# Kernel tuning notes

Hardware: AMD Instinct MI355X
Metric: run time of the kernel (lower is better)

Reference implementation:

```python
import jax, jax.numpy as jnp
import numpy as np

B, S, H = 128, 4096, 128

def setup_inputs() -> dict:
    key = jax.random.key(0)
    k1, k2, k3, k4 = jax.random.split(key, 4)
    x = jax.random.normal(k1, (B, S, H), dtype=jnp.float32)
    # nn.Linear default init ~ U(-1/sqrt(H), 1/sqrt(H)); values don't affect correctness checks
    lim = 1.0 / np.sqrt(H)
    W = jax.random.uniform(k2, (H, H), dtype=jnp.float32, minval=-lim, maxval=lim)
    b = jax.random.uniform(k3, (H,), dtype=jnp.float32, minval=-lim, maxval=lim)
    v = jax.random.uniform(k4, (H,), dtype=jnp.float32, minval=-0.1, maxval=0.1)
    return {"x": x, "W": W, "b": b, "v": v}

def reference(x, W, b, v):
    # score[b,s] = v . tanh(W x[b,s] + b); softmax over series dim S
    h = jnp.tanh(jnp.einsum("bsh,oh->bso", x, W) + b)  # [B,S,H]
    scores = jnp.einsum("bsh,h->bs", h, v)              # [B,S]
    return jax.nn.softmax(scores, axis=-1)
```

## Files before the change

### kernel.cpp

```cpp
#include <hip/hip_runtime.h>
#include <hip/hip_bf16.h>

typedef __attribute__((ext_vector_type(8))) short short8;
typedef __attribute__((ext_vector_type(4))) float f32x4;

#define NB 128
#define NS 4096
#define NH 128
#define NROWS (NB * NS)
#define NSTRIP (NROWS / 16)
#define GRID1 512
#define NWAVES (GRID1 * 4)
#define ITERS (NSTRIP / NWAVES)

static __device__ __forceinline__ short8 pack_bf16x8(f32x4 a, f32x4 b) {
    union { __hip_bfloat162 h[4]; short8 s; } u;
    u.h[0] = __float22bfloat162_rn(make_float2(a[0], a[1]));
    u.h[1] = __float22bfloat162_rn(make_float2(a[2], a[3]));
    u.h[2] = __float22bfloat162_rn(make_float2(b[0], b[1]));
    u.h[3] = __float22bfloat162_rn(make_float2(b[2], b[3]));
    return u.s;
}

static __device__ __forceinline__ float fast_tanh(float z) {
    float e = __builtin_amdgcn_exp2f(z * 2.885390081777927f);
    return 1.0f - 2.0f * __builtin_amdgcn_rcpf(1.0f + e);
}

__global__ __launch_bounds__(256, 2)
void scores_kernel(const float* __restrict__ x, const float* __restrict__ W,
                   const float* __restrict__ bias_p, const float* __restrict__ v_p,
                   float* __restrict__ scores) {
    const int lane = threadIdx.x & 63;
    const int wid  = threadIdx.x >> 6;
    const int col  = lane & 15;
    const int kg   = lane >> 4;

    short8 bf[4][8];
#pragma unroll
    for (int n = 0; n < 8; ++n) {
        const float* wr = W + (n * 16 + col) * NH;
#pragma unroll
        for (int kc = 0; kc < 4; ++kc) {
            f32x4 w0 = *(const f32x4*)(wr + kc * 32 + kg * 8);
            f32x4 w1 = *(const f32x4*)(wr + kc * 32 + kg * 8 + 4);
            bf[kc][n] = pack_bf16x8(w0, w1);
        }
    }
    float bias[8], vv[8];
#pragma unroll
    for (int n = 0; n < 8; ++n) {
        bias[n] = bias_p[n * 16 + col];
        vv[n]   = v_p[n * 16 + col];
    }

    const int gw = blockIdx.x * 4 + wid;
    const float* xp = x + ((long)gw * 16 + col) * NH + kg * 8;
    const long SSTR = (long)NWAVES * 16 * NH;

    f32x4 xl[8];
#pragma unroll
    for (int kc = 0; kc < 4; ++kc) {
        xl[2 * kc]     = *(const f32x4*)(xp + kc * 32);
        xl[2 * kc + 1] = *(const f32x4*)(xp + kc * 32 + 4);
    }

    for (int it = 0; it < ITERS; ++it) {
        short8 a[4];
#pragma unroll
        for (int kc = 0; kc < 4; ++kc) a[kc] = pack_bf16x8(xl[2 * kc], xl[2 * kc + 1]);

        if (it + 1 < ITERS) {
            const float* xn = xp + (long)(it + 1) * SSTR;
#pragma unroll
            for (int kc = 0; kc < 4; ++kc) {
                xl[2 * kc]     = *(const f32x4*)(xn + kc * 32);
                xl[2 * kc + 1] = *(const f32x4*)(xn + kc * 32 + 4);
            }
        }

        f32x4 acc[8];
#pragma unroll
        for (int n = 0; n < 8; ++n) acc[n] = (f32x4){bias[n], bias[n], bias[n], bias[n]};
#pragma unroll
        for (int kc = 0; kc < 4; ++kc)
#pragma unroll
            for (int n = 0; n < 8; ++n)
                acc[n] = __builtin_amdgcn_mfma_f32_16x16x32_bf16(a[kc], bf[kc][n], acc[n], 0, 0, 0);

        float sj[4] = {0.f, 0.f, 0.f, 0.f};
#pragma unroll
        for (int n = 0; n < 8; ++n)
#pragma unroll
            for (int j = 0; j < 4; ++j)
                sj[j] = fmaf(fast_tanh(acc[n][j]), vv[n], sj[j]);

#pragma unroll
        for (int j = 0; j < 4; ++j) {
            sj[j] += __shfl_xor(sj[j], 1);
            sj[j] += __shfl_xor(sj[j], 2);
            sj[j] += __shfl_xor(sj[j], 4);
            sj[j] += __shfl_xor(sj[j], 8);
        }
        if (col < 4) {
            float o = (col == 0) ? sj[0] : (col == 1) ? sj[1] : (col == 2) ? sj[2] : sj[3];
            scores[((long)gw + (long)it * NWAVES) * 16 + kg * 4 + col] = o;
        }
    }
}

__global__ __launch_bounds__(1024)
void softmax_kernel(float* __restrict__ p) {
    float* row = p + (long)blockIdx.x * NS;
    const int t = threadIdx.x;
    const int lane = t & 63, wv = t >> 6;
    f32x4 rv = *(const f32x4*)(row + t * 4);
    f32x4 e;
    float s = 0.f;
#pragma unroll
    for (int i = 0; i < 4; ++i) { e[i] = __expf(rv[i]); s += e[i]; }
#pragma unroll
    for (int d = 1; d < 64; d <<= 1) s += __shfl_xor(s, d);
    __shared__ float red[16];
    if (lane == 0) red[wv] = s;
    __syncthreads();
    float tot = 0.f;
#pragma unroll
    for (int i = 0; i < 16; ++i) tot += red[i];
    float inv = 1.0f / tot;
#pragma unroll
    for (int i = 0; i < 4; ++i) e[i] *= inv;
    *(f32x4*)(row + t * 4) = e;
}

extern "C" void kernel_launch(void* const* d_in, const int* in_sizes, int n_in,
                              void* d_out, int out_size, void* d_ws, size_t ws_size,
                              hipStream_t stream) {
    const float* x = (const float*)d_in[0];
    const float* W = (const float*)d_in[1];
    const float* b = (const float*)d_in[2];
    const float* v = (const float*)d_in[3];
    float* out = (float*)d_out;
    scores_kernel<<<GRID1, 256, 0, stream>>>(x, W, b, v, out);
    softmax_kernel<<<NB, 1024, 0, stream>>>(out);
}
```

Baseline: 59.06 us.

## Stream x strips into per-wave LDS double buffers via global_load_lds

Replaces the one-strip register prefetch of x with direct global-to-LDS loads (global_load_lds) into a per-wave double buffer, keeping two strips in flight. The stored layout is XOR-swizzled to avoid LDS bank conflicts on the read-back. Hand-written s_waitcnt vmcnt values throttle the pipeline. The aim is more outstanding memory traffic and less register pressure in this bandwidth-bound GEMV+tanh pass. It adds 64KB of LDS per block, and it relies on fragile manual counter accounting and on the ordering of LDS reads against the buffer overwrite.

```diff
diff --git a/kernel.cpp b/kernel.cpp
--- a/kernel.cpp
+++ b/kernel.cpp
@@ -27,14 +27,39 @@
     return 1.0f - 2.0f * __builtin_amdgcn_rcpf(1.0f + e);
 }
 
+static __device__ __forceinline__ void gload16(const void* g, const void* lds) {
+    __builtin_amdgcn_global_load_lds(
+        (const unsigned __attribute__((address_space(1)))*)(unsigned long long)g,
+        (unsigned __attribute__((address_space(3)))*)(unsigned)(unsigned long long)lds,
+        16, 0, 0);
+}
+
+static __device__ __forceinline__ void stage_strip(const char* gbase, const char* buf, int lane) {
+#pragma unroll
+    for (int i = 0; i < 8; ++i) {
+        unsigned p = i * 1024 + lane * 16;
+        unsigned src = p ^ (((p >> 9) & 7) << 4);
+        gload16(gbase + src, buf + i * 1024);
+    }
+}
+
 __global__ __launch_bounds__(256, 2)
 void scores_kernel(const float* __restrict__ x, const float* __restrict__ W,
                    const float* __restrict__ bias_p, const float* __restrict__ v_p,
                    float* __restrict__ scores) {
+    __shared__ __align__(16) char smem[65536];
     const int lane = threadIdx.x & 63;
     const int wid  = threadIdx.x >> 6;
     const int col  = lane & 15;
     const int kg   = lane >> 4;
+
+    const int gw = blockIdx.x * 4 + wid;
+    const char* bufb = smem + wid * 16384;
+    const char* xg = (const char*)x + (size_t)gw * 16 * 512;
+    const size_t SBYTES = (size_t)NWAVES * 16 * 512;
+
+    stage_strip(xg, bufb, lane);
+    stage_strip(xg + SBYTES, bufb + 8192, lane);
 
     short8 bf[4][8];
 #pragma unroll
@@ -54,30 +79,28 @@
         vv[n]   = v_p[n * 16 + col];
     }
 
-    const int gw = blockIdx.x * 4 + wid;
-    const float* xp = x + ((long)gw * 16 + col) * NH + kg * 8;
-    const long SSTR = (long)NWAVES * 16 * NH;
+    const int swz = (col & 7) << 4;
 
-    f32x4 xl[8];
-#pragma unroll
-    for (int kc = 0; kc < 4; ++kc) {
-        xl[2 * kc]     = *(const f32x4*)(xp + kc * 32);
-        xl[2 * kc + 1] = *(const f32x4*)(xp + kc * 32 + 4);
-    }
+#pragma unroll 2
+    for (int it = 0; it < ITERS; ++it) {
+        const char* buf = bufb + (it & 1) * 8192;
 
-    for (int it = 0; it < ITERS; ++it) {
+        if (it == 0)              asm volatile("s_waitcnt vmcnt(8)" ::: "memory");
+        else if (it == 1)         asm volatile("s_waitcnt vmcnt(9)" ::: "memory");
+        else if (it == ITERS - 1) asm volatile("s_waitcnt vmcnt(0)" ::: "memory");
+        else                      asm volatile("s_waitcnt vmcnt(10)" ::: "memory");
+
         short8 a[4];
 #pragma unroll
-        for (int kc = 0; kc < 4; ++kc) a[kc] = pack_bf16x8(xl[2 * kc], xl[2 * kc + 1]);
+        for (int kc = 0; kc < 4; ++kc) {
+            const char* rb = buf + col * 512 + kc * 128;
+            f32x4 lo = *(const f32x4*)(rb + ((kg * 32) ^ swz));
+            f32x4 hi = *(const f32x4*)(rb + ((kg * 32 + 16) ^ swz));
+            a[kc] = pack_bf16x8(lo, hi);
+        }
 
-        if (it + 1 < ITERS) {
-            const float* xn = xp + (long)(it + 1) * SSTR;
-#pragma unroll
-            for (int kc = 0; kc < 4; ++kc) {
-                xl[2 * kc]     = *(const f32x4*)(xn + kc * 32);
-                xl[2 * kc + 1] = *(const f32x4*)(xn + kc * 32 + 4);
-            }
-        }
+        if (it + 2 < ITERS)
+            stage_strip(xg + (size_t)(it + 2) * SBYTES, buf, lane);
 
         f32x4 acc[8];
 #pragma unroll
@@ -104,14 +127,14 @@
         }
         if (col < 4) {
             float o = (col == 0) ? sj[0] : (col == 1) ? sj[1] : (col == 2) ? sj[2] : sj[3];
-            scores[((long)gw + (long)it * NWAVES) * 16 + kg * 4 + col] = o;
+            scores[((size_t)gw + (size_t)it * NWAVES) * 16 + kg * 4 + col] = o;
         }
     }
 }
 
 __global__ __launch_bounds__(1024)
 void softmax_kernel(float* __restrict__ p) {
-    float* row = p + (long)blockIdx.x * NS;
+    float* row = p + (size_t)blockIdx.x * NS;
     const int t = threadIdx.x;
     const int lane = t & 63, wv = t >> 6;
     f32x4 rv = *(const f32x4*)(row + t * 4);
```

Result: slower. 60.29 us (+2.1%).
